# Kernel tuning notes

Hardware: AMD Instinct MI355X
Metric: run time of the kernel (lower is better)

Reference implementation:

```python
import jax, jax.numpy as jnp
import numpy as np

N, IN_DIM, OUT_DIM = 16384, 256, 128

def setup_inputs() -> dict:
    key = jax.random.key(0)
    ks = jax.random.split(key, 7)
    s_in = 1.0 / np.sqrt(IN_DIM)
    return {
        "x": jax.random.normal(ks[0], (N, IN_DIM), dtype=jnp.float32),
        "Wq": jax.random.uniform(ks[1], (IN_DIM, OUT_DIM), jnp.float32, -s_in, s_in),
        "bq": jax.random.uniform(ks[2], (OUT_DIM,), jnp.float32, -s_in, s_in),
        "Wk": jax.random.uniform(ks[3], (IN_DIM, OUT_DIM), jnp.float32, -s_in, s_in),
        "bk": jax.random.uniform(ks[4], (OUT_DIM,), jnp.float32, -s_in, s_in),
        "Wv": jax.random.uniform(ks[5], (IN_DIM, OUT_DIM), jnp.float32, -s_in, s_in),
        "bv": jax.random.uniform(ks[6], (OUT_DIM,), jnp.float32, -s_in, s_in),
    }

def reference(x, Wq, bq, Wk, bk, Wv, bv):
    # QKV projections: [N, out_dim]
    q = x @ Wq + bq
    k = x @ Wk + bk
    v = x @ Wv + bv
    # Unscaled dot-product affinity [N, N], row softmax, weighted sum of V.
    affinity = jax.nn.softmax(q @ k.T, axis=-1)
    return affinity @ v
```

## Files before the change

kernel.cpp:

```cpp
#include <hip/hip_runtime.h>

typedef _Float16 f16;
typedef _Float16 f16x8 __attribute__((ext_vector_type(8)));
typedef _Float16 f16x4 __attribute__((ext_vector_type(4)));
typedef float f32x4 __attribute__((ext_vector_type(4)));
typedef float f32x16 __attribute__((ext_vector_type(16)));
typedef unsigned uint2v __attribute__((ext_vector_type(2)));

#define MFMA16(a, b, c) __builtin_amdgcn_mfma_f32_16x16x32_f16((a), (b), (c), 0, 0, 0)
#define MFMA32(a, b, c) __builtin_amdgcn_mfma_f32_32x32x16_f16((a), (b), (c), 0, 0, 0)
#define LOG2E 1.44269504088896340736f
#define SHIFT_L2 28.8539008178f

#define GLOAD_LDS16(g, l)                                              \
    __builtin_amdgcn_global_load_lds(                                  \
        (const __attribute__((address_space(1))) void*)(g),            \
        (__attribute__((address_space(3))) void*)(l), 16, 0, 0)

#define NROWS 16384
#define INDIM 256
#define ODIM 128
#define NQT 128
#define BN 32

__global__ __launch_bounds__(256) void prep_kernel(
    const float* __restrict__ Wq, const float* __restrict__ Wk, const float* __restrict__ Wv,
    f16* __restrict__ WqT, f16* __restrict__ WkT, f16* __restrict__ WvT) {
    int w = blockIdx.x >> 5;
    int local = blockIdx.x & 31;
    const float* W = (w == 0) ? Wq : ((w == 1) ? Wk : Wv);
    f16* WT = (w == 0) ? WqT : ((w == 1) ? WkT : WvT);
    int j0 = local * 1024 + threadIdx.x;
#pragma unroll
    for (int t = 0; t < 4; t++) {
        int j = j0 + t * 256;
        int n = j >> 8;
        int k = j & 255;
        WT[j] = (f16)W[k * ODIM + n];
    }
}

__global__ __launch_bounds__(256) void proj_kernel(
    const float* __restrict__ x,
    const f16* __restrict__ WqT, const f16* __restrict__ WkT, const f16* __restrict__ WvT,
    const float* __restrict__ bq, const float* __restrict__ bk, const float* __restrict__ bv,
    f16* __restrict__ Qh, f16* __restrict__ Kh, f16* __restrict__ Vt) {
    int blk = blockIdx.x;
    int wave = threadIdx.x >> 6;
    int lane = threadIdx.x & 63;
    int l16 = lane & 15, quad = lane >> 4;

    int r0 = (blk & 255) * 64 + wave * 16;
    int c0 = (blk >> 8) * 64;

    f16x8 ax[8];
    const float* xp = x + (size_t)(r0 + l16) * INDIM + quad * 8;
#pragma unroll
    for (int kc = 0; kc < 8; kc++) {
        f32x4 u = *(const f32x4*)(xp + kc * 32);
        f32x4 v = *(const f32x4*)(xp + kc * 32 + 4);
        f16x8 t;
        t[0] = (f16)u[0]; t[1] = (f16)u[1]; t[2] = (f16)u[2]; t[3] = (f16)u[3];
        t[4] = (f16)v[0]; t[5] = (f16)v[1]; t[6] = (f16)v[2]; t[7] = (f16)v[3];
        ax[kc] = t;
    }
#pragma unroll
    for (int nt = 0; nt < 4; nt++) {
        int colb = c0 + nt * 16;
        f32x4 aq = {0.f, 0.f, 0.f, 0.f}, ak = {0.f, 0.f, 0.f, 0.f};
        f32x4 av = {0.f, 0.f, 0.f, 0.f};
        const f16* wq = WqT + (colb + l16) * INDIM + quad * 8;
        const f16* wk = WkT + (colb + l16) * INDIM + quad * 8;
        const f16* wv = WvT + (colb + l16) * INDIM + quad * 8;
#pragma unroll
        for (int kc = 0; kc < 8; kc++) {
            f16x8 bqf = *(const f16x8*)(wq + kc * 32);
            f16x8 bkf = *(const f16x8*)(wk + kc * 32);
            f16x8 avf = *(const f16x8*)(wv + kc * 32);
            aq = MFMA16(ax[kc], bqf, aq);
            ak = MFMA16(ax[kc], bkf, ak);
            av = MFMA16(avf, ax[kc], av);
        }
        int col = colb + l16;
        float biasq = bq[col], biask = bk[col];
#pragma unroll
        for (int r = 0; r < 4; r++) {
            int row = r0 + quad * 4 + r;
            Qh[(size_t)row * ODIM + col] = (f16)(aq[r] + biasq);
            Kh[(size_t)row * ODIM + col] = (f16)(ak[r] + biask);
            int d = colb + quad * 4 + r;
            Vt[(size_t)d * NROWS + r0 + l16] = (f16)(av[r] + bv[d]);
        }
    }
}

__global__ __launch_bounds__(256, 4) void flash_kernel(
    const f16* __restrict__ Qh, const f16* __restrict__ Kh, const f16* __restrict__ Vt,
    f16* __restrict__ Opart, float* __restrict__ lbuf, float* __restrict__ Out,
    int nsplit, int niter) {
    int blk = blockIdx.x;
    int qt = blk & (NQT - 1);
    int sp = blk >> 7;
    int tid = threadIdx.x;
    int wave = tid >> 6;
    int lane = tid & 63;
    int l32 = lane & 31;
    int h = lane >> 5;

    __shared__ __align__(16) f16 Kl[2][BN * 128];
    __shared__ __align__(16) f16 Vl[2][128 * BN];

    int rowbase = qt * 128 + wave * 32;

    f16x8 qf[8];
    {
        const f16* qp = Qh + (size_t)(rowbase + l32) * ODIM + h * 8;
#pragma unroll
        for (int ks = 0; ks < 8; ks++) qf[ks] = *(const f16x8*)(qp + ks * 16);
    }

    f32x16 o[4];
#pragma unroll
    for (int dt = 0; dt < 4; dt++)
#pragma unroll
        for (int g = 0; g < 16; g++) o[dt][g] = 0.f;
    float l_r = 0.f;

    int rK[2], cK[2], dV[2], cV[2];
#pragma unroll
    for (int t = 0; t < 2; t++) {
        int s = wave * 128 + t * 64 + lane;
        rK[t] = s >> 4;
        cK[t] = ((s & 15) ^ (rK[t] & 7)) * 8;
        dV[t] = s >> 2;
        cV[t] = ((s & 3) ^ ((dV[t] >> 1) & 3)) * 8;
    }
    int rr = (l32 >> 1) & 3;
    int hh = h ^ (l32 & 1);
    int vh = h ^ ((l32 >> 1) & 1);
    int vk = (l32 >> 2) & 1;

    int j0 = sp * (niter * BN);

#pragma unroll
    for (int t = 0; t < 2; t++) {
        GLOAD_LDS16(Kh + (size_t)(j0 + rK[t]) * ODIM + cK[t],
                    &Kl[0][(wave * 2 + t) * 512]);
        GLOAD_LDS16(Vt + (size_t)dV[t] * NROWS + j0 + cV[t],
                    &Vl[0][(wave * 2 + t) * 512]);
    }
    __syncthreads();

    for (int it = 0; it < niter; ++it) {
        int p = it & 1;
        if (it + 1 < niter) {
            int jn = j0 + BN;
#pragma unroll
            for (int t = 0; t < 2; t++) {
                GLOAD_LDS16(Kh + (size_t)(jn + rK[t]) * ODIM + cK[t],
                            &Kl[1 - p][(wave * 2 + t) * 512]);
                GLOAD_LDS16(Vt + (size_t)dV[t] * NROWS + jn + cV[t],
                            &Vl[1 - p][(wave * 2 + t) * 512]);
            }
        }
        int pk[8];
        {
            f32x16 st;
#pragma unroll
            for (int g = 0; g < 16; g++) st[g] = 0.f;
            const f16* kb = &Kl[p][l32 * 128 + hh * 8];
            __builtin_amdgcn_s_setprio(1);
#pragma unroll
            for (int ks = 0; ks < 8; ks++) {
                f16x8 kf = *(const f16x8*)(kb + ((ks ^ rr) << 4));
                st = MFMA32(kf, qf[ks], st);
            }
            __builtin_amdgcn_s_setprio(0);
#pragma unroll
            for (int w = 0; w < 8; w++) {
                float a = __builtin_amdgcn_exp2f(fmaf(st[2 * w], LOG2E, -SHIFT_L2));
                float b = __builtin_amdgcn_exp2f(fmaf(st[2 * w + 1], LOG2E, -SHIFT_L2));
                l_r += a + b;
                pk[w] = __builtin_bit_cast(int, __builtin_amdgcn_cvt_pkrtz(a, b));
            }
        }
        f16x8 pf[2];
#if __has_builtin(__builtin_amdgcn_permlane32_swap)
#pragma unroll
        for (int ks = 0; ks < 2; ks++) {
            int b = ks * 4;
            uint2v r02 = __builtin_amdgcn_permlane32_swap(
                (unsigned)pk[b], (unsigned)pk[b + 2], false, false);
            uint2v r13 = __builtin_amdgcn_permlane32_swap(
                (unsigned)pk[b + 1], (unsigned)pk[b + 3], false, false);
            union { unsigned i[4]; f16x8 v; } u;
            u.i[0] = r02.x;
            u.i[1] = r13.x;
            u.i[2] = r02.y;
            u.i[3] = r13.y;
            pf[ks] = u.v;
        }
#else
#pragma unroll
        for (int ks = 0; ks < 2; ks++) {
            int b = ks * 4;
            int off0 = h ? pk[b] : pk[b + 2];
            int off1 = h ? pk[b + 1] : pk[b + 3];
            int R0 = __shfl_xor(off0, 32, 64);
            int R1 = __shfl_xor(off1, 32, 64);
            union { int i[4]; f16x8 v; } u;
            u.i[0] = h ? R0 : pk[b];
            u.i[1] = h ? R1 : pk[b + 1];
            u.i[2] = h ? pk[b + 2] : R0;
            u.i[3] = h ? pk[b + 3] : R1;
            pf[ks] = u.v;
        }
#endif
        __builtin_amdgcn_s_setprio(1);
#pragma unroll
        for (int dt = 0; dt < 4; dt++) {
            const f16* vb = &Vl[p][(dt * 32 + l32) * BN + vh * 8];
#pragma unroll
            for (int ks = 0; ks < 2; ks++) {
                f16x8 vf = *(const f16x8*)(vb + ((ks ^ vk) << 4));
                o[dt] = MFMA32(vf, pf[ks], o[dt]);
            }
        }
        __builtin_amdgcn_s_setprio(0);
        __syncthreads();
        j0 += BN;
    }

    l_r += __shfl_xor(l_r, 32, 64);

    if (nsplit == 1) {
        float inv = 1.f / l_r;
        float* op = Out + (size_t)(rowbase + l32) * ODIM;
#pragma unroll
        for (int dt = 0; dt < 4; dt++)
#pragma unroll
            for (int gg = 0; gg < 4; gg++) {
                f32x4 v = {o[dt][4 * gg] * inv, o[dt][4 * gg + 1] * inv,
                           o[dt][4 * gg + 2] * inv, o[dt][4 * gg + 3] * inv};
                *(f32x4*)(op + dt * 32 + 8 * gg + 4 * h) = v;
            }
    } else {
        f16* op = Opart + ((size_t)sp * NROWS + rowbase + l32) * ODIM;
#pragma unroll
        for (int dt = 0; dt < 4; dt++)
#pragma unroll
            for (int gg = 0; gg < 4; gg++) {
                f16x4 v = {(f16)o[dt][4 * gg], (f16)o[dt][4 * gg + 1],
                           (f16)o[dt][4 * gg + 2], (f16)o[dt][4 * gg + 3]};
                *(f16x4*)(op + dt * 32 + 8 * gg + 4 * h) = v;
            }
        if (lane < 32)
            lbuf[(size_t)sp * NROWS + rowbase + l32] = l_r;
    }
}

__global__ __launch_bounds__(256) void merge_kernel(const f16* __restrict__ Opart,
                                                    const float* __restrict__ lbuf,
                                                    float* __restrict__ out, int nsplit) {
    int idx = (blockIdx.x * 256 + threadIdx.x) * 4;
    int row = idx >> 7;
    f32x4 acc = {0.f, 0.f, 0.f, 0.f};
    float den = 0.f;
    for (int s = 0; s < nsplit; s++) {
        f16x4 v = *(const f16x4*)(Opart + (size_t)s * (NROWS * ODIM) + idx);
        acc[0] += (float)v[0]; acc[1] += (float)v[1];
        acc[2] += (float)v[2]; acc[3] += (float)v[3];
        den += lbuf[(size_t)s * NROWS + row];
    }
    float inv = 1.f / den;
    f32x4 r = {acc[0] * inv, acc[1] * inv, acc[2] * inv, acc[3] * inv};
    *(f32x4*)(out + idx) = r;
}

extern "C" void kernel_launch(void* const* d_in, const int* in_sizes, int n_in,
                              void* d_out, int out_size, void* d_ws, size_t ws_size,
                              hipStream_t stream) {
    const float* x  = (const float*)d_in[0];
    const float* Wq = (const float*)d_in[1];
    const float* bq = (const float*)d_in[2];
    const float* Wk = (const float*)d_in[3];
    const float* bk = (const float*)d_in[4];
    const float* Wv = (const float*)d_in[5];
    const float* bv = (const float*)d_in[6];
    float* out = (float*)d_out;
    char* ws = (char*)d_ws;

    const size_t WT_BYTES = (size_t)ODIM * INDIM * sizeof(f16);
    const size_t QKV_BYTES = (size_t)NROWS * ODIM * sizeof(f16);
    f16* WqT = (f16*)(ws);
    f16* WkT = (f16*)(ws + WT_BYTES);
    f16* WvT = (f16*)(ws + 2 * WT_BYTES);
    f16* Qh  = (f16*)(ws + 3 * WT_BYTES);
    f16* Kh  = (f16*)(ws + 3 * WT_BYTES + QKV_BYTES);
    f16* Vt  = (f16*)(ws + 3 * WT_BYTES + 2 * QKV_BYTES);
    size_t base = 3 * WT_BYTES + 3 * QKV_BYTES;

    const size_t OPART_BYTES = (size_t)NROWS * ODIM * sizeof(f16);
    const size_t L_BYTES = (size_t)NROWS * sizeof(float);

    int nsplit = 1;
    if (ws_size >= base + 8 * (OPART_BYTES + L_BYTES)) nsplit = 8;
    else if (ws_size >= base + 4 * (OPART_BYTES + L_BYTES)) nsplit = 4;
    else if (ws_size >= base + 2 * (OPART_BYTES + L_BYTES)) nsplit = 2;

    f16* Opart = (f16*)(ws + base);
    float* lbuf = (float*)(ws + base + (size_t)nsplit * OPART_BYTES);

    prep_kernel<<<96, 256, 0, stream>>>(Wq, Wk, Wv, WqT, WkT, WvT);
    proj_kernel<<<512, 256, 0, stream>>>(x, WqT, WkT, WvT, bq, bk, bv, Qh, Kh, Vt);
    flash_kernel<<<NQT * nsplit, 256, 0, stream>>>(Qh, Kh, Vt, Opart, lbuf, out, nsplit,
                                                   (NROWS / BN) / nsplit);
    if (nsplit > 1)
        merge_kernel<<<(NROWS * ODIM) / 1024, 256, 0, stream>>>(Opart, lbuf, out, nsplit);
}
```

Baseline: 294.6 us.

## Triple-buffer K/V tiles with partial vmcnt waits and reduce split-K to 4

Moves the flash kernel's K/V LDS staging from double to triple buffering, prefetching two tiles ahead. The full __syncthreads is replaced by s_waitcnt vmcnt(4) plus s_barrier, so only the oldest tile's loads must land before the next iteration. This is meant to hide global-load latency. It also caps nsplit at 4 instead of 8, which halves the grid, doubles per-block iterations and cuts merge traffic. The cost is more LDS per block, which may lower occupancy, and fewer blocks to fill the CUs.

```diff
diff --git a/kernel.cpp b/kernel.cpp
--- a/kernel.cpp
+++ b/kernel.cpp
@@ -22,6 +22,7 @@
 #define ODIM 128
 #define NQT 128
 #define BN 32
+#define NBUF 3
 
 __global__ __launch_bounds__(256) void prep_kernel(
     const float* __restrict__ Wq, const float* __restrict__ Wk, const float* __restrict__ Wv,
@@ -107,8 +108,8 @@
     int l32 = lane & 31;
     int h = lane >> 5;
 
-    __shared__ __align__(16) f16 Kl[2][BN * 128];
-    __shared__ __align__(16) f16 Vl[2][128 * BN];
+    __shared__ __align__(16) f16 Kl[NBUF][BN * 128];
+    __shared__ __align__(16) f16 Vl[NBUF][128 * BN];
 
     int rowbase = qt * 128 + wave * 32;
 
@@ -149,18 +150,29 @@
         GLOAD_LDS16(Vt + (size_t)dV[t] * NROWS + j0 + cV[t],
                     &Vl[0][(wave * 2 + t) * 512]);
     }
-    __syncthreads();
+#pragma unroll
+    for (int t = 0; t < 2; t++) {
+        GLOAD_LDS16(Kh + (size_t)(j0 + BN + rK[t]) * ODIM + cK[t],
+                    &Kl[1][(wave * 2 + t) * 512]);
+        GLOAD_LDS16(Vt + (size_t)dV[t] * NROWS + j0 + BN + cV[t],
+                    &Vl[1][(wave * 2 + t) * 512]);
+    }
+    asm volatile("s_waitcnt vmcnt(4)" ::: "memory");
+    __builtin_amdgcn_s_barrier();
+    __builtin_amdgcn_sched_barrier(0);
+
+    int cur = 0;
+    int bd = 2;
 
     for (int it = 0; it < niter; ++it) {
-        int p = it & 1;
-        if (it + 1 < niter) {
-            int jn = j0 + BN;
+        if (it + 2 < niter) {
+            int jn = j0 + 2 * BN;
 #pragma unroll
             for (int t = 0; t < 2; t++) {
                 GLOAD_LDS16(Kh + (size_t)(jn + rK[t]) * ODIM + cK[t],
-                            &Kl[1 - p][(wave * 2 + t) * 512]);
+                            &Kl[bd][(wave * 2 + t) * 512]);
                 GLOAD_LDS16(Vt + (size_t)dV[t] * NROWS + jn + cV[t],
-                            &Vl[1 - p][(wave * 2 + t) * 512]);
+                            &Vl[bd][(wave * 2 + t) * 512]);
             }
         }
         int pk[8];
@@ -168,7 +180,7 @@
             f32x16 st;
 #pragma unroll
             for (int g = 0; g < 16; g++) st[g] = 0.f;
-            const f16* kb = &Kl[p][l32 * 128 + hh * 8];
+            const f16* kb = &Kl[cur][l32 * 128 + hh * 8];
             __builtin_amdgcn_s_setprio(1);
 #pragma unroll
             for (int ks = 0; ks < 8; ks++) {
@@ -219,7 +231,7 @@
         __builtin_amdgcn_s_setprio(1);
 #pragma unroll
         for (int dt = 0; dt < 4; dt++) {
-            const f16* vb = &Vl[p][(dt * 32 + l32) * BN + vh * 8];
+            const f16* vb = &Vl[cur][(dt * 32 + l32) * BN + vh * 8];
 #pragma unroll
             for (int ks = 0; ks < 2; ks++) {
                 f16x8 vf = *(const f16x8*)(vb + ((ks ^ vk) << 4));
@@ -227,7 +239,15 @@
             }
         }
         __builtin_amdgcn_s_setprio(0);
-        __syncthreads();
+        if (it + 2 < niter) {
+            asm volatile("s_waitcnt vmcnt(4)" ::: "memory");
+        } else {
+            asm volatile("s_waitcnt vmcnt(0)" ::: "memory");
+        }
+        __builtin_amdgcn_s_barrier();
+        __builtin_amdgcn_sched_barrier(0);
+        cur = (cur == NBUF - 1) ? 0 : cur + 1;
+        bd = (bd == NBUF - 1) ? 0 : bd + 1;
         j0 += BN;
     }
 
@@ -304,8 +324,7 @@
     const size_t L_BYTES = (size_t)NROWS * sizeof(float);
 
     int nsplit = 1;
-    if (ws_size >= base + 8 * (OPART_BYTES + L_BYTES)) nsplit = 8;
-    else if (ws_size >= base + 4 * (OPART_BYTES + L_BYTES)) nsplit = 4;
+    if (ws_size >= base + 4 * (OPART_BYTES + L_BYTES)) nsplit = 4;
     else if (ws_size >= base + 2 * (OPART_BYTES + L_BYTES)) nsplit = 2;
 
     f16* Opart = (f16*)(ws + base);
```

New measurement: 278.2 us. 5.6% less time.

## Enlarge flash tiles to 256 query rows and 64 keys per iteration

Applied to the files above, without the earlier changes.

The flash kernel now runs 512-thread blocks (8 waves) that each cover 256 query rows, and it processes 64 keys per iteration instead of 32, with a new LDS swizzle for the wider V tile. Each staged K/V tile is shared by twice as many query rows and the loop runs half as many iterations, which cuts global loads and barriers per unit of work. In exchange the LDS footprint doubles, the register pressure from the two score tiles grows, and the grid has half as many blocks, which may lower occupancy or balance across CUs.

```diff
diff --git a/kernel.cpp b/kernel.cpp
--- a/kernel.cpp
+++ b/kernel.cpp
@@ -20,8 +20,8 @@
 #define NROWS 16384
 #define INDIM 256
 #define ODIM 128
-#define NQT 128
-#define BN 32
+#define NQT 64
+#define BN 64
 
 __global__ __launch_bounds__(256) void prep_kernel(
     const float* __restrict__ Wq, const float* __restrict__ Wk, const float* __restrict__ Wv,
@@ -94,13 +94,13 @@
     }
 }
 
-__global__ __launch_bounds__(256, 4) void flash_kernel(
+__global__ __launch_bounds__(512, 4) void flash_kernel(
     const f16* __restrict__ Qh, const f16* __restrict__ Kh, const f16* __restrict__ Vt,
     f16* __restrict__ Opart, float* __restrict__ lbuf, float* __restrict__ Out,
     int nsplit, int niter) {
     int blk = blockIdx.x;
     int qt = blk & (NQT - 1);
-    int sp = blk >> 7;
+    int sp = blk >> 6;
     int tid = threadIdx.x;
     int wave = tid >> 6;
     int lane = tid & 63;
@@ -110,7 +110,7 @@
     __shared__ __align__(16) f16 Kl[2][BN * 128];
     __shared__ __align__(16) f16 Vl[2][128 * BN];
 
-    int rowbase = qt * 128 + wave * 32;
+    int rowbase = qt * 256 + wave * 32;
 
     f16x8 qf[8];
     {
@@ -132,13 +132,11 @@
         int s = wave * 128 + t * 64 + lane;
         rK[t] = s >> 4;
         cK[t] = ((s & 15) ^ (rK[t] & 7)) * 8;
-        dV[t] = s >> 2;
-        cV[t] = ((s & 3) ^ ((dV[t] >> 1) & 3)) * 8;
+        dV[t] = s >> 3;
+        cV[t] = ((s & 7) ^ (dV[t] & 7)) * 8;
     }
     int rr = (l32 >> 1) & 3;
     int hh = h ^ (l32 & 1);
-    int vh = h ^ ((l32 >> 1) & 1);
-    int vk = (l32 >> 2) & 1;
 
     int j0 = sp * (niter * BN);
 
@@ -163,12 +161,13 @@
                             &Vl[1 - p][(wave * 2 + t) * 512]);
             }
         }
-        int pk[8];
-        {
+        int pk[2][8];
+#pragma unroll
+        for (int ct = 0; ct < 2; ct++) {
             f32x16 st;
 #pragma unroll
             for (int g = 0; g < 16; g++) st[g] = 0.f;
-            const f16* kb = &Kl[p][l32 * 128 + hh * 8];
+            const f16* kb = &Kl[p][(ct * 32 + l32) * 128 + hh * 8];
             __builtin_amdgcn_s_setprio(1);
 #pragma unroll
             for (int ks = 0; ks < 8; ks++) {
@@ -181,18 +180,18 @@
                 float a = __builtin_amdgcn_exp2f(fmaf(st[2 * w], LOG2E, -SHIFT_L2));
                 float b = __builtin_amdgcn_exp2f(fmaf(st[2 * w + 1], LOG2E, -SHIFT_L2));
                 l_r += a + b;
-                pk[w] = __builtin_bit_cast(int, __builtin_amdgcn_cvt_pkrtz(a, b));
-            }
-        }
-        f16x8 pf[2];
+                pk[ct][w] = __builtin_bit_cast(int, __builtin_amdgcn_cvt_pkrtz(a, b));
+            }
+        }
+        f16x8 pf[4];
 #if __has_builtin(__builtin_amdgcn_permlane32_swap)
 #pragma unroll
-        for (int ks = 0; ks < 2; ks++) {
-            int b = ks * 4;
+        for (int ks = 0; ks < 4; ks++) {
+            int ct = ks >> 1, b = (ks & 1) * 4;
             uint2v r02 = __builtin_amdgcn_permlane32_swap(
-                (unsigned)pk[b], (unsigned)pk[b + 2], false, false);
+                (unsigned)pk[ct][b], (unsigned)pk[ct][b + 2], false, false);
             uint2v r13 = __builtin_amdgcn_permlane32_swap(
-                (unsigned)pk[b + 1], (unsigned)pk[b + 3], false, false);
+                (unsigned)pk[ct][b + 1], (unsigned)pk[ct][b + 3], false, false);
             union { unsigned i[4]; f16x8 v; } u;
             u.i[0] = r02.x;
             u.i[1] = r13.x;
@@ -202,27 +201,27 @@
         }
 #else
 #pragma unroll
-        for (int ks = 0; ks < 2; ks++) {
-            int b = ks * 4;
-            int off0 = h ? pk[b] : pk[b + 2];
-            int off1 = h ? pk[b + 1] : pk[b + 3];
+        for (int ks = 0; ks < 4; ks++) {
+            int ct = ks >> 1, b = (ks & 1) * 4;
+            int off0 = h ? pk[ct][b] : pk[ct][b + 2];
+            int off1 = h ? pk[ct][b + 1] : pk[ct][b + 3];
             int R0 = __shfl_xor(off0, 32, 64);
             int R1 = __shfl_xor(off1, 32, 64);
             union { int i[4]; f16x8 v; } u;
-            u.i[0] = h ? R0 : pk[b];
-            u.i[1] = h ? R1 : pk[b + 1];
-            u.i[2] = h ? pk[b + 2] : R0;
-            u.i[3] = h ? pk[b + 3] : R1;
+            u.i[0] = h ? R0 : pk[ct][b];
+            u.i[1] = h ? R1 : pk[ct][b + 1];
+            u.i[2] = h ? pk[ct][b + 2] : R0;
+            u.i[3] = h ? pk[ct][b + 3] : R1;
             pf[ks] = u.v;
         }
 #endif
         __builtin_amdgcn_s_setprio(1);
 #pragma unroll
         for (int dt = 0; dt < 4; dt++) {
-            const f16* vb = &Vl[p][(dt * 32 + l32) * BN + vh * 8];
-#pragma unroll
-            for (int ks = 0; ks < 2; ks++) {
-                f16x8 vf = *(const f16x8*)(vb + ((ks ^ vk) << 4));
+            const f16* vb = &Vl[p][(dt * 32 + l32) * 64 + hh * 8];
+#pragma unroll
+            for (int ks = 0; ks < 4; ks++) {
+                f16x8 vf = *(const f16x8*)(vb + ((ks ^ rr) << 4));
                 o[dt] = MFMA32(vf, pf[ks], o[dt]);
             }
         }
@@ -313,7 +312,7 @@
 
     prep_kernel<<<96, 256, 0, stream>>>(Wq, Wk, Wv, WqT, WkT, WvT);
     proj_kernel<<<512, 256, 0, stream>>>(x, WqT, WkT, WvT, bq, bk, bv, Qh, Kh, Vt);
-    flash_kernel<<<NQT * nsplit, 256, 0, stream>>>(Qh, Kh, Vt, Opart, lbuf, out, nsplit,
+    flash_kernel<<<NQT * nsplit, 512, 0, stream>>>(Qh, Kh, Vt, Opart, lbuf, out, nsplit,
                                                    (NROWS / BN) / nsplit);
     if (nsplit > 1)
         merge_kernel<<<(NROWS * ODIM) / 1024, 256, 0, stream>>>(Opart, lbuf, out, nsplit);
```

Result: slower. 353.1 us (+19.9%).
